# Kernel optimization log

Hardware: AMD Instinct MI355X
Metric: run time of the kernel (lower is better)

Reference implementation:

```python
import jax, jax.numpy as jnp
import numpy as np

B, S, IN, OUT = 64, 512, 256, 256   # batch, seq_len, in/out features
R, NB, E = 40, 3, 262144            # num_rels, num_bases, num_edges
N = B * S                           # total nodes in batched graph


def setup_inputs() -> dict:
    key = jax.random.key(0)
    ks = jax.random.split(key, 6)
    text = jax.random.normal(ks[0], (B, S, IN), jnp.float32)
    src = jax.random.randint(ks[1], (E,), 0, N)
    dst = jax.random.randint(ks[2], (E,), 0, N)
    rel = jax.random.randint(ks[3], (E,), 0, R)
    bases = jax.random.normal(ks[4], (NB, IN, OUT), jnp.float32) / np.sqrt(IN).astype(np.float32)
    comp = jax.random.normal(ks[5], (R, NB), jnp.float32)
    bias = jnp.zeros((OUT,), jnp.float32)
    return dict(text=text, src=src, dst=dst, rel=rel, bases=bases, comp=comp, bias=bias)


def reference(text, src, dst, rel, bases, comp, bias):
    Bt, St, INt = text.shape
    h = text.reshape(-1, INt)                       # [N, in] flattened node feats
    n_nodes = h.shape[0]
    # project every node through every basis once: [N, num_bases, out]
    t = jnp.einsum('ni,bio->nbo', h, bases)
    # per-edge message: sum_b comp[rel_e, b] * (h_src @ basis_b)  -> [E, out]
    msg = jnp.einsum('eb,ebo->eo', comp[rel], t[src])
    # scatter-sum aggregation to destination nodes
    agg = jax.ops.segment_sum(msg, dst, num_segments=n_nodes)   # [N, out]
    out = jax.nn.relu(agg + bias)
    return out.reshape(Bt, -1, out.shape[-1])
```

## Files before the change

kernel.cpp:

```cpp
#include <hip/hip_runtime.h>
#include <cstdint>

#define N_NODES 32768
#define IN_F    256
#define OUT_F   256
#define NBASES  3
#define N_EDGES 262144
#define K_DIM   (NBASES * IN_F)

typedef __attribute__((ext_vector_type(8))) short bf16x8;
typedef __attribute__((ext_vector_type(4))) float f32x4;

__device__ __forceinline__ unsigned short f2bf(float x) {
    union { float f; unsigned int u; } c; c.f = x;
    unsigned int u = c.u;
    u = (u + 0x7FFFu + ((u >> 16) & 1u)) >> 16;
    return (unsigned short)u;
}
__device__ __forceinline__ float bf2f(unsigned short h) {
    union { unsigned int u; float f; } c; c.u = ((unsigned int)h) << 16;
    return c.f;
}

__device__ __forceinline__ void async_copy16(const void* g, void* l) {
    __builtin_amdgcn_global_load_lds(
        (const __attribute__((address_space(1))) unsigned int*)g,
        (__attribute__((address_space(3))) unsigned int*)l, 16, 0, 0);
}

__global__ __launch_bounds__(256) void prep_kernel(
    const float* __restrict__ text,
    const float* __restrict__ bases,
    unsigned short* __restrict__ hb,
    unsigned short* __restrict__ Wt,
    int* __restrict__ counts)
{
    const int tid = threadIdx.x;
    if (blockIdx.x < 8192) {
        int i = blockIdx.x * 256 + tid;
        float4 v = reinterpret_cast<const float4*>(text)[i];
        ushort4 o;
        o.x = f2bf(v.x); o.y = f2bf(v.y); o.z = f2bf(v.z); o.w = f2bf(v.w);
        reinterpret_cast<ushort4*>(hb)[i] = o;
    } else if (blockIdx.x < 8384) {
        int tb = blockIdx.x - 8192;
        int kb = tb % 24, ob = tb / 24;
        __shared__ float tile[32][33];
        int c = tid & 31, r8 = tid >> 5;
        #pragma unroll
        for (int i = 0; i < 4; ++i) {
            int r = r8 + 8 * i;
            tile[r][c] = bases[(size_t)(kb * 32 + r) * OUT_F + ob * 32 + c];
        }
        __syncthreads();
        #pragma unroll
        for (int i = 0; i < 4; ++i) {
            int r = r8 + 8 * i;
            Wt[(size_t)(ob * 32 + r) * K_DIM + kb * 32 + c] = f2bf(tile[c][r]);
        }
    } else {
        int i = (blockIdx.x - 8384) * 256 + tid;
        counts[i] = 0;
    }
}

__global__ __launch_bounds__(256) void hist_kernel(
    const int* __restrict__ dst, int* __restrict__ counts)
{
    int e4 = blockIdx.x * 256 + threadIdx.x;
    int4 d = reinterpret_cast<const int4*>(dst)[e4];
    atomicAdd(&counts[d.x], 1);
    atomicAdd(&counts[d.y], 1);
    atomicAdd(&counts[d.z], 1);
    atomicAdd(&counts[d.w], 1);
}

__global__ __launch_bounds__(1024) void scan_kernel(
    int* __restrict__ counts,
    int* __restrict__ offsets)
{
    __shared__ int wsum[16];
    const int tid = threadIdx.x;
    const int wave = tid >> 6, lane = tid & 63;
    const int base = tid * 32;
    int local[32];
    int sum = 0;
    #pragma unroll
    for (int k8 = 0; k8 < 8; ++k8) {
        int4 v = reinterpret_cast<const int4*>(counts + base)[k8];
        local[k8 * 4 + 0] = v.x; local[k8 * 4 + 1] = v.y;
        local[k8 * 4 + 2] = v.z; local[k8 * 4 + 3] = v.w;
        sum += v.x + v.y + v.z + v.w;
    }
    int inc = sum;
    #pragma unroll
    for (int off = 1; off < 64; off <<= 1) {
        int v = __shfl_up(inc, off);
        if (lane >= off) inc += v;
    }
    if (lane == 63) wsum[wave] = inc;
    __syncthreads();
    if (wave == 0 && lane < 16) {
        int v = wsum[lane];
        #pragma unroll
        for (int off = 1; off < 16; off <<= 1) {
            int u = __shfl_up(v, off);
            if (lane >= off) v += u;
        }
        wsum[lane] = v;
    }
    __syncthreads();
    int run = inc - sum + (wave ? wsum[wave - 1] : 0);
    #pragma unroll
    for (int k = 0; k < 32; ++k) {
        offsets[base + k] = run;
        counts[base + k] = run;
        run += local[k];
    }
    if (tid == 1023) offsets[N_NODES] = run;
}

__global__ __launch_bounds__(256) void scatter_kernel(
    const int* __restrict__ dst, const int* __restrict__ src,
    const int* __restrict__ rel, const float* __restrict__ comp,
    int* __restrict__ cursor, int2* __restrict__ packed2)
{
    int e4 = blockIdx.x * 256 + threadIdx.x;
    int4 d = reinterpret_cast<const int4*>(dst)[e4];
    int4 s = reinterpret_cast<const int4*>(src)[e4];
    int4 r = reinterpret_cast<const int4*>(rel)[e4];
    int dd[4] = { d.x, d.y, d.z, d.w };
    int ss[4] = { s.x, s.y, s.z, s.w };
    int rr[4] = { r.x, r.y, r.z, r.w };
    #pragma unroll
    for (int q = 0; q < 4; ++q) {
        float c0 = comp[rr[q] * 3 + 0];
        float c1 = comp[rr[q] * 3 + 1];
        float c2 = comp[rr[q] * 3 + 2];
        int w0 = ss[q] | ((int)f2bf(c0) << 16);
        int w1 = (int)f2bf(c1) | ((int)f2bf(c2) << 16);
        int pos = atomicAdd(&cursor[dd[q]], 1);
        packed2[pos] = make_int2(w0, w1);
    }
}

__global__ __launch_bounds__(256) void agg_kernel(
    const unsigned short* __restrict__ hb,
    const int2* __restrict__ packed2,
    const int* __restrict__ offsets,
    unsigned short* __restrict__ z)
{
    const int node = blockIdx.x * 4 + (threadIdx.x >> 6);
    const int lane = threadIdx.x & 63;
    const int start = offsets[node];
    const int end   = offsets[node + 1];

    float a0[4] = {}, a1[4] = {}, a2[4] = {};
    const unsigned short* hp = hb + lane * 4;

    for (int cb = start; cb < end; cb += 64) {
        int idx = cb + lane;
        int wx = 0, wy = 0;
        if (idx < end) { int2 w = packed2[idx]; wx = w.x; wy = w.y; }
        int cnt = min(64, end - cb);
        for (int j = 0; j < cnt; j += 8) {
            float c0[8], c1[8], c2[8];
            ushort4 u[8];
            #pragma unroll
            for (int q = 0; q < 8; ++q) {
                int p0 = __shfl(wx, j + q);
                int p1 = __shfl(wy, j + q);
                int s = p0 & 0xFFFF;
                float m = (j + q < cnt) ? 1.f : 0.f;
                c0[q] = m * bf2f((unsigned short)((unsigned)p0 >> 16));
                c1[q] = m * bf2f((unsigned short)(p1 & 0xFFFF));
                c2[q] = m * bf2f((unsigned short)((unsigned)p1 >> 16));
                u[q] = *reinterpret_cast<const ushort4*>(hp + (size_t)s * IN_F);
            }
            #pragma unroll
            for (int q = 0; q < 8; ++q) {
                float v[4] = { bf2f(u[q].x), bf2f(u[q].y),
                               bf2f(u[q].z), bf2f(u[q].w) };
                #pragma unroll
                for (int k = 0; k < 4; ++k) {
                    a0[k] += c0[q] * v[k];
                    a1[k] += c1[q] * v[k];
                    a2[k] += c2[q] * v[k];
                }
            }
        }
    }

    unsigned short* zp = z + (size_t)node * K_DIM + lane * 4;
    ushort4 o;
    o.x = f2bf(a0[0]); o.y = f2bf(a0[1]); o.z = f2bf(a0[2]); o.w = f2bf(a0[3]);
    *reinterpret_cast<ushort4*>(zp) = o;
    o.x = f2bf(a1[0]); o.y = f2bf(a1[1]); o.z = f2bf(a1[2]); o.w = f2bf(a1[3]);
    *reinterpret_cast<ushort4*>(zp + 256) = o;
    o.x = f2bf(a2[0]); o.y = f2bf(a2[1]); o.z = f2bf(a2[2]); o.w = f2bf(a2[3]);
    *reinterpret_cast<ushort4*>(zp + 512) = o;
}

__global__ __launch_bounds__(256) void gemm_kernel(
    const unsigned short* __restrict__ A,
    const unsigned short* __restrict__ Bt,
    const float* __restrict__ bias,
    float* __restrict__ out)
{
    __shared__ __align__(16) unsigned short As[2][128 * 32];
    __shared__ __align__(16) unsigned short Bs[2][128 * 32];

    const int tid  = threadIdx.x;
    const int wave = tid >> 6, lane = tid & 63;
    const int quad = lane >> 4, l16 = lane & 15;
    const int wm = (wave & 1) * 64, wn = (wave >> 1) * 64;
    const int m0 = blockIdx.x * 128, n0 = blockIdx.y * 128;

    f32x4 acc[4][4] = {};

    const unsigned short *ga[2], *gb[2];
    int lab[2];
    #pragma unroll
    for (int c = 0; c < 2; ++c) {
        int p = c * 256 + wave * 64 + lane;
        int row = p >> 2;
        int oct = (p & 3) ^ ((row >> 1) & 3);
        ga[c] = A  + (size_t)(m0 + row) * K_DIM + oct * 8;
        gb[c] = Bt + (size_t)(n0 + row) * K_DIM + oct * 8;
        lab[c] = (c * 256 + wave * 64) * 8;
    }

    #pragma unroll
    for (int c = 0; c < 2; ++c) {
        async_copy16(ga[c], &As[0][lab[c]]);
        async_copy16(gb[c], &Bs[0][lab[c]]);
    }

    int cur = 0;
    for (int step = 0; step < K_DIM / 32; ++step) {
        __syncthreads();
        int k1 = (step + 1) * 32;
        if (k1 < K_DIM) {
            #pragma unroll
            for (int c = 0; c < 2; ++c) {
                async_copy16(ga[c] + k1, &As[cur ^ 1][lab[c]]);
                async_copy16(gb[c] + k1, &Bs[cur ^ 1][lab[c]]);
            }
        }

        bf16x8 af[4], bfr[4];
        #pragma unroll
        for (int i = 0; i < 4; ++i) {
            int row = wm + i * 16 + l16;
            int oph = quad ^ ((row >> 1) & 3);
            af[i] = *reinterpret_cast<const bf16x8*>(&As[cur][(row * 4 + oph) * 8]);
            int nn   = wn + i * 16 + l16;
            int oph2 = quad ^ ((nn >> 1) & 3);
            bfr[i] = *reinterpret_cast<const bf16x8*>(&Bs[cur][(nn * 4 + oph2) * 8]);
        }
        #pragma unroll
        for (int i = 0; i < 4; ++i)
            #pragma unroll
            for (int j = 0; j < 4; ++j)
                acc[i][j] = __builtin_amdgcn_mfma_f32_16x16x32_bf16(
                    af[i], bfr[j], acc[i][j], 0, 0, 0);
        cur ^= 1;
    }

    #pragma unroll
    for (int j = 0; j < 4; ++j) {
        int col = n0 + wn + j * 16 + l16;
        float bv = bias[col];
        #pragma unroll
        for (int i = 0; i < 4; ++i) {
            int row_base = m0 + wm + i * 16 + quad * 4;
            #pragma unroll
            for (int r = 0; r < 4; ++r)
                out[(size_t)(row_base + r) * OUT_F + col] =
                    fmaxf(acc[i][j][r] + bv, 0.f);
        }
    }
}

extern "C" void kernel_launch(void* const* d_in, const int* in_sizes, int n_in,
                              void* d_out, int out_size, void* d_ws, size_t ws_size,
                              hipStream_t stream) {
    const float* text  = (const float*)d_in[0];
    const int*   src   = (const int*)d_in[1];
    const int*   dst   = (const int*)d_in[2];
    const int*   rel   = (const int*)d_in[3];
    const float* bases = (const float*)d_in[4];
    const float* comp  = (const float*)d_in[5];
    const float* bias  = (const float*)d_in[6];
    float* out = (float*)d_out;

    char* p = (char*)d_ws;
    unsigned short* z  = (unsigned short*)p;      p += (size_t)N_NODES * K_DIM * 2;
    unsigned short* hb = (unsigned short*)p;      p += (size_t)N_NODES * IN_F * 2;
    int2* packed2 = (int2*)p;                     p += (size_t)N_EDGES * 8;
    int* offsets  = (int*)p;                      p += (size_t)(N_NODES + 4) * 4;
    int* counts   = (int*)p;                      p += (size_t)N_NODES * 4;
    unsigned short* Wt = (unsigned short*)p;

    prep_kernel<<<8512, 256, 0, stream>>>(text, bases, hb, Wt, counts);
    hist_kernel<<<N_EDGES / 1024, 256, 0, stream>>>(dst, counts);
    scan_kernel<<<1, 1024, 0, stream>>>(counts, offsets);
    scatter_kernel<<<N_EDGES / 1024, 256, 0, stream>>>(
        dst, src, rel, comp, counts, packed2);
    agg_kernel<<<N_NODES / 4, 256, 0, stream>>>(hb, packed2, offsets, z);
    gemm_kernel<<<dim3(N_NODES / 128, OUT_F / 128), 256, 0, stream>>>(
        z, Wt, bias, out);
}
```

Before: 185.0 us.

## Load GEMM MFMA fragments directly from global memory, dropping LDS staging

The GEMM kernel no longer stages A and B tiles through double-buffered shared memory with async global-to-LDS copies. Each wave now loads its MFMA operand fragments straight from global memory into registers, prefetching the next K slice one step ahead. This removes the block barriers and the LDS traffic, but each wave re-reads data that other waves in the block share. Global and L2 traffic goes up, and loads become 16-byte accesses strided across rows.

```diff
diff --git a/kernel.cpp b/kernel.cpp
--- a/kernel.cpp
+++ b/kernel.cpp
@@ -20,12 +20,6 @@
 __device__ __forceinline__ float bf2f(unsigned short h) {
     union { unsigned int u; float f; } c; c.u = ((unsigned int)h) << 16;
     return c.f;
-}
-
-__device__ __forceinline__ void async_copy16(const void* g, void* l) {
-    __builtin_amdgcn_global_load_lds(
-        (const __attribute__((address_space(1))) unsigned int*)g,
-        (__attribute__((address_space(3))) unsigned int*)l, 16, 0, 0);
 }
 
 __global__ __launch_bounds__(256) void prep_kernel(
@@ -207,9 +201,6 @@
     const float* __restrict__ bias,
     float* __restrict__ out)
 {
-    __shared__ __align__(16) unsigned short As[2][128 * 32];
-    __shared__ __align__(16) unsigned short Bs[2][128 * 32];
-
     const int tid  = threadIdx.x;
     const int wave = tid >> 6, lane = tid & 63;
     const int quad = lane >> 4, l16 = lane & 15;
@@ -218,53 +209,34 @@
 
     f32x4 acc[4][4] = {};
 
-    const unsigned short *ga[2], *gb[2];
-    int lab[2];
-    #pragma unroll
-    for (int c = 0; c < 2; ++c) {
-        int p = c * 256 + wave * 64 + lane;
-        int row = p >> 2;
-        int oct = (p & 3) ^ ((row >> 1) & 3);
-        ga[c] = A  + (size_t)(m0 + row) * K_DIM + oct * 8;
-        gb[c] = Bt + (size_t)(n0 + row) * K_DIM + oct * 8;
-        lab[c] = (c * 256 + wave * 64) * 8;
-    }
-
-    #pragma unroll
-    for (int c = 0; c < 2; ++c) {
-        async_copy16(ga[c], &As[0][lab[c]]);
-        async_copy16(gb[c], &Bs[0][lab[c]]);
-    }
-
-    int cur = 0;
-    for (int step = 0; step < K_DIM / 32; ++step) {
-        __syncthreads();
-        int k1 = (step + 1) * 32;
-        if (k1 < K_DIM) {
-            #pragma unroll
-            for (int c = 0; c < 2; ++c) {
-                async_copy16(ga[c] + k1, &As[cur ^ 1][lab[c]]);
-                async_copy16(gb[c] + k1, &Bs[cur ^ 1][lab[c]]);
-            }
-        }
-
-        bf16x8 af[4], bfr[4];
-        #pragma unroll
-        for (int i = 0; i < 4; ++i) {
-            int row = wm + i * 16 + l16;
-            int oph = quad ^ ((row >> 1) & 3);
-            af[i] = *reinterpret_cast<const bf16x8*>(&As[cur][(row * 4 + oph) * 8]);
-            int nn   = wn + i * 16 + l16;
-            int oph2 = quad ^ ((nn >> 1) & 3);
-            bfr[i] = *reinterpret_cast<const bf16x8*>(&Bs[cur][(nn * 4 + oph2) * 8]);
+    const unsigned short* ap = A  + (size_t)(m0 + wm + l16) * K_DIM + quad * 8;
+    const unsigned short* bp = Bt + (size_t)(n0 + wn + l16) * K_DIM + quad * 8;
+
+    bf16x8 a0[4], b0[4];
+    #pragma unroll
+    for (int i = 0; i < 4; ++i) {
+        a0[i] = *reinterpret_cast<const bf16x8*>(ap + (size_t)i * 16 * K_DIM);
+        b0[i] = *reinterpret_cast<const bf16x8*>(bp + (size_t)i * 16 * K_DIM);
+    }
+
+    for (int c = 0; c < K_DIM / 32; ++c) {
+        int off = (c + 1 < K_DIM / 32 ? c + 1 : c) * 32;
+        bf16x8 a1[4], b1[4];
+        #pragma unroll
+        for (int i = 0; i < 4; ++i) {
+            a1[i] = *reinterpret_cast<const bf16x8*>(
+                ap + (size_t)i * 16 * K_DIM + off);
+            b1[i] = *reinterpret_cast<const bf16x8*>(
+                bp + (size_t)i * 16 * K_DIM + off);
         }
         #pragma unroll
         for (int i = 0; i < 4; ++i)
             #pragma unroll
             for (int j = 0; j < 4; ++j)
                 acc[i][j] = __builtin_amdgcn_mfma_f32_16x16x32_bf16(
-                    af[i], bfr[j], acc[i][j], 0, 0, 0);
-        cur ^= 1;
+                    a0[i], b0[j], acc[i][j], 0, 0, 0);
+        #pragma unroll
+        for (int i = 0; i < 4; ++i) { a0[i] = a1[i]; b0[i] = b1[i]; }
     }
 
     #pragma unroll
```

New measurement: 205.9 us. 1.11x slower.
